# Performance work log

Measured on AMD Instinct MI355X. Metric: run time of the kernel, lower is better.

The kernel has to match this reference:

```python
import jax, jax.numpy as jnp
import numpy as np

TREE_DEPTH = 3
CONSTANTS = jnp.array([-1.0, 0.0, 1.0], dtype=jnp.float32)


def setup_inputs() -> dict:
    key = jax.random.key(0)
    ks = jax.random.split(key, 5)
    B, S, D, W, SLOT = 2, 2048, 1024, 4096, 8
    C = SLOT + 3
    hidden = jax.random.normal(ks[0], (B, S, D), dtype=jnp.float32)
    slot_w = jax.random.normal(ks[1], (D, SLOT), dtype=jnp.float32) * (0.5 / np.sqrt(D))
    slot_b = jnp.zeros((SLOT,), dtype=jnp.float32)
    leaf_logits = jax.random.normal(ks[2], (W, 1 << TREE_DEPTH, C), dtype=jnp.float32) * 0.02
    node_params = jnp.array([1.0, 1.0, 0.25, 0.0, 0.0], dtype=jnp.float32)
    out_w = jax.random.normal(ks[3], (W, D), dtype=jnp.float32) * (0.5 / np.sqrt(W))
    out_b = jnp.zeros((D,), dtype=jnp.float32)
    return {"hidden": hidden, "slot_w": slot_w, "slot_b": slot_b,
            "leaf_logits": leaf_logits, "node_params": node_params,
            "out_w": out_w, "out_b": out_b}


def reference(hidden, slot_w, slot_b, leaf_logits, node_params, out_w, out_b):
    B, S, _ = hidden.shape
    # basis: tanh slot projection concatenated with fixed constants -> [B,S,slot+3]
    slots = jnp.tanh(hidden @ slot_w + slot_b)
    consts = jnp.broadcast_to(CONSTANTS.astype(hidden.dtype), (B, S, 3))
    basis = jnp.concatenate((slots, consts), axis=-1)
    # leaf values: softmax-weighted mixture over the tiny basis dim -> [B,S,W,leaf]
    selector = jax.nn.softmax(leaf_logits.astype(hidden.dtype), axis=-1)
    values = jnp.einsum('wlc,bsc->bswl', selector, basis)
    lw, rw, pw, dw, nb = [p.astype(hidden.dtype) for p in node_params]
    for _ in range(TREE_DEPTH):
        left, right = values[..., 0::2], values[..., 1::2]
        values = jnp.tanh(lw * left + rw * right + pw * left * right
                          + dw * (left - right) + nb)
    roots = values[..., 0]  # [B,S,W]
    return roots @ out_w + out_b
```

## Files before the change

kernel.cpp:

```cpp
#include <hip/hip_runtime.h>
#include <stdint.h>

#define BSZ   4096
#define DIM   1024
#define WTR   4096
#define KDIM  4096
#define W8    32768

typedef unsigned short u16;
typedef __attribute__((ext_vector_type(8))) short bhalf8;
typedef __attribute__((ext_vector_type(4))) float floatx4;
typedef __attribute__((ext_vector_type(16))) float floatx16;

__device__ __forceinline__ u16 f2bf(float f) {
    union { float f; uint32_t i; } v; v.f = f;
    uint32_t r = v.i + 0x7fffu + ((v.i >> 16) & 1u);
    return (u16)(r >> 16);
}
__device__ __forceinline__ float fast_tanh(float x) {
    float e = __builtin_amdgcn_exp2f(x * 2.885390081777927f);
    return fmaf(-2.0f, __builtin_amdgcn_rcpf(e + 1.0f), 1.0f);
}
__device__ __forceinline__ void load16(const void* g, void* lds) {
    __builtin_amdgcn_global_load_lds(
        (const __attribute__((address_space(1))) uint32_t*)g,
        (__attribute__((address_space(3))) uint32_t*)lds, 16, 0, 0);
}

__global__ __launch_bounds__(256) void k_prep(const float* __restrict__ ll,
                                              u16* __restrict__ selwA,
                                              const float* __restrict__ ow,
                                              u16* __restrict__ owt,
                                              const float* __restrict__ slot_w,
                                              u16* __restrict__ swT) {
    int bid = blockIdx.x, tid = threadIdx.x;
    if (bid < 128) {
        int row = bid * 256 + tid;
        int w = row >> 3, l = row & 7, q = w & 3;
        int prow = (w >> 2) * 32 + (l & 3) + 8 * (l >> 2) + 16 * (q & 1) + 4 * (q >> 1);
        const float* p = ll + (size_t)row * 11;
        float v[11]; float m = -1e30f;
        #pragma unroll
        for (int c = 0; c < 11; ++c) { v[c] = p[c]; m = fmaxf(m, v[c]); }
        float s = 0.f;
        #pragma unroll
        for (int c = 0; c < 11; ++c) {
            v[c] = __builtin_amdgcn_exp2f((v[c] - m) * 1.4426950408889634f);
            s += v[c];
        }
        float inv = __builtin_amdgcn_rcpf(s);
        union { u16 h[16]; uint4 qq[2]; } o;
        #pragma unroll
        for (int c = 0; c < 8; ++c) o.h[c] = f2bf(v[c] * inv);
        o.h[8] = f2bf((v[10] - v[8]) * inv);
        #pragma unroll
        for (int c = 9; c < 16; ++c) o.h[c] = 0;
        uint4* dst = (uint4*)(selwA + (size_t)prow * 16);
        dst[0] = o.qq[0]; dst[1] = o.qq[1];
    } else if (bid < 128 + 4096) {
        int b = bid - 128;
        int d0 = (b & 31) * 32, w0 = (b >> 5) * 32;
        int tx = tid & 31, ty = tid >> 5;
        __shared__ float tile[32][33];
        #pragma unroll
        for (int i = 0; i < 32; i += 8)
            tile[ty + i][tx] = ow[(size_t)(w0 + ty + i) * DIM + d0 + tx];
        __syncthreads();
        #pragma unroll
        for (int i = 0; i < 32; i += 8)
            owt[(size_t)(d0 + ty + i) * WTR + w0 + tx] = f2bf(tile[tx][ty + i]);
    } else {
        int b = bid - 128 - 4096;
        for (int it = 0; it < 8; ++it) {
            int idx = b * 2048 + it * 256 + tid;
            int s = idx >> 10, d = idx & 1023;
            float val = (s < 8) ? slot_w[(size_t)d * 8 + s] : 0.f;
            swT[(size_t)s * DIM + d] = f2bf(val);
        }
    }
}

__global__ __launch_bounds__(256) void k_basis(const float* __restrict__ hidden,
                                               const u16* __restrict__ swT,
                                               const float* __restrict__ slot_b,
                                               u16* __restrict__ basisTB) {
    int m0 = blockIdx.x * 16;
    int tid = threadIdx.x, lane = tid & 63, wid = tid >> 6;
    int col = lane & 15, quad = lane >> 4;
    const float* ga = hidden + (size_t)(m0 + col) * DIM + wid * 256 + quad * 8;
    const u16*   gb = swT + (size_t)col * DIM + wid * 256 + quad * 8;
    floatx4 acc = (floatx4){0.f, 0.f, 0.f, 0.f};
    #pragma unroll
    for (int k0 = 0; k0 < 256; k0 += 32) {
        float4 a0 = *(const float4*)(ga + k0);
        float4 a1 = *(const float4*)(ga + k0 + 4);
        bhalf8 bf = *(const bhalf8*)(gb + k0);
        bhalf8 af;
        af[0] = (short)f2bf(a0.x); af[1] = (short)f2bf(a0.y);
        af[2] = (short)f2bf(a0.z); af[3] = (short)f2bf(a0.w);
        af[4] = (short)f2bf(a1.x); af[5] = (short)f2bf(a1.y);
        af[6] = (short)f2bf(a1.z); af[7] = (short)f2bf(a1.w);
        acc = __builtin_amdgcn_mfma_f32_16x16x32_bf16(af, bf, acc, 0, 0, 0);
    }
    __shared__ float smr[4][16][16];
    #pragma unroll
    for (int r = 0; r < 4; ++r) smr[wid][quad * 4 + r][col] = acc[r];
    __syncthreads();
    int tt = tid >> 4, cc = tid & 15;
    float s = smr[0][tt][cc] + smr[1][tt][cc] + smr[2][tt][cc] + smr[3][tt][cc];
    u16 val;
    if (cc < 8)       val = f2bf(fast_tanh(s + slot_b[cc]));
    else if (cc == 8) val = (u16)0x3f80;
    else              val = 0;
    basisTB[(size_t)(m0 + tt) * 16 + cc] = val;
}

__device__ __forceinline__ float tree_eval(float v[8], float lw, float rw,
                                           float pw, float dw, float nb) {
    #pragma unroll
    for (int lev = 0; lev < 3; ++lev) {
        int n = 4 >> lev;
        #pragma unroll
        for (int i = 0; i < 4; ++i) {
            if (i < n) {
                float L = v[2*i], R = v[2*i+1];
                float x = fmaf(lw, L, nb);
                x = fmaf(rw, R, x);
                x = fmaf(pw, L * R, x);
                x = fmaf(dw, L - R, x);
                v[i] = fast_tanh(x);
            }
        }
    }
    return v[0];
}

__global__ __launch_bounds__(256, 2) void k_roots(const u16* __restrict__ selwA,
                                                  const u16* __restrict__ basisTB,
                                                  const float* __restrict__ np_,
                                                  u16* __restrict__ roots) {
    __shared__ uint32_t st[4][32 * 12];
    int tid = threadIdx.x, wid = tid >> 6, lane = tid & 63;
    int c = lane & 31, h = lane >> 5;
    int tile0 = blockIdx.x * 16 + wid * 4;
    int w0w   = tile0 * 4;
    int t0b   = blockIdx.y * 512;
    float lw = np_[0], rw = np_[1], pw = np_[2], dw = np_[3], nb = np_[4];

    bhalf8 af[4];
    #pragma unroll
    for (int tl = 0; tl < 4; ++tl)
        af[tl] = *(const bhalf8*)(selwA + (size_t)((tile0 + tl) * 32 + c) * 16 + h * 8);

    uint32_t* myst = st[wid];
    for (int it = 0; it < 16; ++it) {
        int t0 = t0b + it * 32;
        bhalf8 bf = *(const bhalf8*)(basisTB + (size_t)(t0 + c) * 16 + h * 8);
        #pragma unroll
        for (int tl = 0; tl < 4; ++tl) {
            floatx16 z = {0.f,0.f,0.f,0.f,0.f,0.f,0.f,0.f,
                          0.f,0.f,0.f,0.f,0.f,0.f,0.f,0.f};
            floatx16 cc = __builtin_amdgcn_mfma_f32_32x32x16_bf16(af[tl], bf, z, 0, 0, 0);
            float vA[8], vB[8];
            #pragma unroll
            for (int l = 0; l < 8; ++l) { vA[l] = cc[l]; vB[l] = cc[8 + l]; }
            float rA = tree_eval(vA, lw, rw, pw, dw, nb);
            float rB = tree_eval(vB, lw, rw, pw, dw, nb);
            myst[c * 12 + tl * 2 + h] = (uint32_t)f2bf(rA) | ((uint32_t)f2bf(rB) << 16);
        }
        __syncthreads();
        uint4 q = *(const uint4*)(myst + c * 12 + h * 4);
        *(uint4*)(roots + (size_t)(t0 + c) * WTR + w0w + h * 8) = q;
        __syncthreads();
    }
}

__global__ __launch_bounds__(256) void k_gemm(const u16* __restrict__ A,
                                              const u16* __restrict__ Bt,
                                              const float* __restrict__ out_b,
                                              float* __restrict__ C) {
    __shared__ __align__(16) u16 smA[2][64 * 64];
    __shared__ __align__(16) u16 smB[2][128 * 64];
    int tid = threadIdx.x;
    int bm = blockIdx.x * 64, bn = blockIdx.y * 128;
    int lane = tid & 63, wid = tid >> 6;
    int wm = (wid >> 1) * 32, wn = (wid & 1) * 64;

    floatx4 acc[2][4];
    #pragma unroll
    for (int i = 0; i < 2; ++i)
        #pragma unroll
        for (int j = 0; j < 4; ++j) acc[i][j] = (floatx4){0.f, 0.f, 0.f, 0.f};

    int ar = tid >> 3;
    int ak = ((tid & 7) ^ (ar & 7)) * 8;
    const u16* gA = A  + (size_t)(bm + ar) * KDIM + ak;
    const u16* gB = Bt + (size_t)(bn + ar) * KDIM + ak;

    int col = lane & 15, quad = lane >> 4, csw = col & 7;

    {
        char* ldA = (char*)smA[0] + tid * 16;
        char* ldB = (char*)smB[0] + tid * 16;
        load16(gA,                       ldA);
        load16(gA + (size_t)32 * KDIM,   ldA + 4096);
        load16(gB,                       ldB);
        load16(gB + (size_t)32 * KDIM,   ldB + 4096);
        load16(gB + (size_t)64 * KDIM,   ldB + 8192);
        load16(gB + (size_t)96 * KDIM,   ldB + 12288);
        gA += 64; gB += 64;
    }

    int cur = 0;
    for (int k0 = 0; k0 < KDIM / 64; ++k0) {
        __syncthreads();
        if (k0 < KDIM / 64 - 1) {
            char* ldA = (char*)smA[cur ^ 1] + tid * 16;
            char* ldB = (char*)smB[cur ^ 1] + tid * 16;
            load16(gA,                       ldA);
            load16(gA + (size_t)32 * KDIM,   ldA + 4096);
            load16(gB,                       ldB);
            load16(gB + (size_t)32 * KDIM,   ldB + 4096);
            load16(gB + (size_t)64 * KDIM,   ldB + 8192);
            load16(gB + (size_t)96 * KDIM,   ldB + 12288);
            gA += 64; gB += 64;
        }
        const u16* sa = smA[cur];
        const u16* sb = smB[cur];
        #pragma unroll
        for (int kk = 0; kk < 2; ++kk) {
            int kc = kk * 4 + quad;
            bhalf8 af[2], bf[4];
            #pragma unroll
            for (int i = 0; i < 2; ++i)
                af[i] = *(const bhalf8*)(sa + ((wm + i * 16 + col) * 8 + (kc ^ csw)) * 8);
            #pragma unroll
            for (int j = 0; j < 4; ++j)
                bf[j] = *(const bhalf8*)(sb + ((wn + j * 16 + col) * 8 + (kc ^ csw)) * 8);
            #pragma unroll
            for (int i = 0; i < 2; ++i)
                #pragma unroll
                for (int j = 0; j < 4; ++j)
                    acc[i][j] = __builtin_amdgcn_mfma_f32_16x16x32_bf16(
                        af[i], bf[j], acc[i][j], 0, 0, 0);
        }
        cur ^= 1;
    }

    #pragma unroll
    for (int j = 0; j < 4; ++j) {
        int n = bn + wn + j * 16 + col;
        float bv = out_b[n];
        #pragma unroll
        for (int i = 0; i < 2; ++i) {
            int m0 = bm + wm + i * 16 + quad * 4;
            #pragma unroll
            for (int r = 0; r < 4; ++r)
                C[(size_t)(m0 + r) * DIM + n] = acc[i][j][r] + bv;
        }
    }
}

extern "C" void kernel_launch(void* const* d_in, const int* in_sizes, int n_in,
                              void* d_out, int out_size, void* d_ws, size_t ws_size,
                              hipStream_t stream) {
    const float* hidden      = (const float*)d_in[0];
    const float* slot_w      = (const float*)d_in[1];
    const float* slot_b      = (const float*)d_in[2];
    const float* leaf_logits = (const float*)d_in[3];
    const float* node_params = (const float*)d_in[4];
    const float* out_w       = (const float*)d_in[5];
    const float* out_b       = (const float*)d_in[6];
    float* out = (float*)d_out;

    char* ws = (char*)d_ws;
    u16* selwA   = (u16*)ws;
    u16* basisTB = (u16*)(ws + 1048576);
    u16* swT     = (u16*)(ws + 1179648);
    u16* outwt   = (u16*)(ws + 1212416);
    u16* roots   = (u16*)(ws + 9601024);

    k_prep <<<128 + 4096 + 8, 256, 0, stream>>>(leaf_logits, selwA, out_w, outwt, slot_w, swT);
    k_basis<<<BSZ / 16, 256, 0, stream>>>(hidden, swT, slot_b, basisTB);
    k_roots<<<dim3(64, 8), 256, 0, stream>>>(selwA, basisTB, node_params, roots);
    k_gemm <<<dim3(BSZ / 64, DIM / 128), 256, 0, stream>>>(roots, outwt, out_b, out);
}
```

Measured before the change: 206.8 us.

## Split-K final GEMM with atomic accumulation and coalesce roots stores

The output GEMM is split into two K halves across grid z, and each half accumulates into an output that k_prep pre-initializes with the bias, using atomicAdd. The GEMM drops LDS double buffering in favor of a single buffer with two barriers per step. k_roots now stages all four waves' results into a shared padded, double-buffered LDS tile, so each token row is written as one contiguous 128-byte segment and one barrier per iteration is removed. The aim is more blocks in flight for the GEMM and better-coalesced stores, at the cost of atomic traffic, nondeterministic summation order and less load/compute overlap in the GEMM.

```diff
diff --git a/kernel.cpp b/kernel.cpp
--- a/kernel.cpp
+++ b/kernel.cpp
@@ -32,7 +32,9 @@
                                               const float* __restrict__ ow,
                                               u16* __restrict__ owt,
                                               const float* __restrict__ slot_w,
-                                              u16* __restrict__ swT) {
+                                              u16* __restrict__ swT,
+                                              const float* __restrict__ out_b,
+                                              float* __restrict__ C) {
     int bid = blockIdx.x, tid = threadIdx.x;
     if (bid < 128) {
         int row = bid * 256 + tid;
@@ -69,13 +71,21 @@
         #pragma unroll
         for (int i = 0; i < 32; i += 8)
             owt[(size_t)(d0 + ty + i) * WTR + w0 + tx] = f2bf(tile[tx][ty + i]);
-    } else {
+    } else if (bid < 128 + 4096 + 8) {
         int b = bid - 128 - 4096;
         for (int it = 0; it < 8; ++it) {
             int idx = b * 2048 + it * 256 + tid;
             int s = idx >> 10, d = idx & 1023;
             float val = (s < 8) ? slot_w[(size_t)d * 8 + s] : 0.f;
             swT[(size_t)s * DIM + d] = f2bf(val);
+        }
+    } else {
+        int b = bid - 128 - 4096 - 8;
+        float4 bv = *(const float4*)(out_b + (tid & 255) * 4);
+        #pragma unroll
+        for (int it = 0; it < 16; ++it) {
+            size_t flat = (size_t)b * 16384 + it * 1024 + (tid & 255) * 4;
+            *(float4*)(C + flat) = bv;
         }
     }
 }
@@ -139,11 +149,11 @@
                                                   const u16* __restrict__ basisTB,
                                                   const float* __restrict__ np_,
                                                   u16* __restrict__ roots) {
-    __shared__ uint32_t st[4][32 * 12];
+    __shared__ uint32_t st[2][32 * 33];
     int tid = threadIdx.x, wid = tid >> 6, lane = tid & 63;
     int c = lane & 31, h = lane >> 5;
     int tile0 = blockIdx.x * 16 + wid * 4;
-    int w0w   = tile0 * 4;
+    int wblk  = blockIdx.x * 64;
     int t0b   = blockIdx.y * 512;
     float lw = np_[0], rw = np_[1], pw = np_[2], dw = np_[3], nb = np_[4];
 
@@ -152,9 +162,10 @@
     for (int tl = 0; tl < 4; ++tl)
         af[tl] = *(const bhalf8*)(selwA + (size_t)((tile0 + tl) * 32 + c) * 16 + h * 8);
 
-    uint32_t* myst = st[wid];
+    int tok = tid >> 3, ch = tid & 7;
     for (int it = 0; it < 16; ++it) {
         int t0 = t0b + it * 32;
+        uint32_t* buf = st[it & 1];
         bhalf8 bf = *(const bhalf8*)(basisTB + (size_t)(t0 + c) * 16 + h * 8);
         #pragma unroll
         for (int tl = 0; tl < 4; ++tl) {
@@ -166,23 +177,27 @@
             for (int l = 0; l < 8; ++l) { vA[l] = cc[l]; vB[l] = cc[8 + l]; }
             float rA = tree_eval(vA, lw, rw, pw, dw, nb);
             float rB = tree_eval(vB, lw, rw, pw, dw, nb);
-            myst[c * 12 + tl * 2 + h] = (uint32_t)f2bf(rA) | ((uint32_t)f2bf(rB) << 16);
-        }
-        __syncthreads();
-        uint4 q = *(const uint4*)(myst + c * 12 + h * 4);
-        *(uint4*)(roots + (size_t)(t0 + c) * WTR + w0w + h * 8) = q;
-        __syncthreads();
+            buf[c * 33 + wid * 8 + tl * 2 + h] =
+                (uint32_t)f2bf(rA) | ((uint32_t)f2bf(rB) << 16);
+        }
+        __syncthreads();
+        uint32_t d0 = buf[tok * 33 + ch * 4];
+        uint32_t d1 = buf[tok * 33 + ch * 4 + 1];
+        uint32_t d2 = buf[tok * 33 + ch * 4 + 2];
+        uint32_t d3 = buf[tok * 33 + ch * 4 + 3];
+        uint4 q; q.x = d0; q.y = d1; q.z = d2; q.w = d3;
+        *(uint4*)(roots + (size_t)(t0 + tok) * WTR + wblk + ch * 8) = q;
     }
 }
 
 __global__ __launch_bounds__(256) void k_gemm(const u16* __restrict__ A,
                                               const u16* __restrict__ Bt,
-                                              const float* __restrict__ out_b,
                                               float* __restrict__ C) {
-    __shared__ __align__(16) u16 smA[2][64 * 64];
-    __shared__ __align__(16) u16 smB[2][128 * 64];
+    __shared__ __align__(16) u16 smA[64 * 64];
+    __shared__ __align__(16) u16 smB[128 * 64];
     int tid = threadIdx.x;
     int bm = blockIdx.x * 64, bn = blockIdx.y * 128;
+    int koff = blockIdx.z * (KDIM / 2);
     int lane = tid & 63, wid = tid >> 6;
     int wm = (wid >> 1) * 32, wn = (wid & 1) * 64;
 
@@ -194,14 +209,15 @@
 
     int ar = tid >> 3;
     int ak = ((tid & 7) ^ (ar & 7)) * 8;
-    const u16* gA = A  + (size_t)(bm + ar) * KDIM + ak;
-    const u16* gB = Bt + (size_t)(bn + ar) * KDIM + ak;
+    const u16* gA = A  + (size_t)(bm + ar) * KDIM + koff + ak;
+    const u16* gB = Bt + (size_t)(bn + ar) * KDIM + koff + ak;
+    char* ldA = (char*)smA + tid * 16;
+    char* ldB = (char*)smB + tid * 16;
 
     int col = lane & 15, quad = lane >> 4, csw = col & 7;
 
-    {
-        char* ldA = (char*)smA[0] + tid * 16;
-        char* ldB = (char*)smB[0] + tid * 16;
+    for (int k0 = 0; k0 < KDIM / 2 / 64; ++k0) {
+        __syncthreads();
         load16(gA,                       ldA);
         load16(gA + (size_t)32 * KDIM,   ldA + 4096);
         load16(gB,                       ldB);
@@ -209,34 +225,18 @@
         load16(gB + (size_t)64 * KDIM,   ldB + 8192);
         load16(gB + (size_t)96 * KDIM,   ldB + 12288);
         gA += 64; gB += 64;
-    }
-
-    int cur = 0;
-    for (int k0 = 0; k0 < KDIM / 64; ++k0) {
-        __syncthreads();
-        if (k0 < KDIM / 64 - 1) {
-            char* ldA = (char*)smA[cur ^ 1] + tid * 16;
-            char* ldB = (char*)smB[cur ^ 1] + tid * 16;
-            load16(gA,                       ldA);
-            load16(gA + (size_t)32 * KDIM,   ldA + 4096);
-            load16(gB,                       ldB);
-            load16(gB + (size_t)32 * KDIM,   ldB + 4096);
-            load16(gB + (size_t)64 * KDIM,   ldB + 8192);
-            load16(gB + (size_t)96 * KDIM,   ldB + 12288);
-            gA += 64; gB += 64;
-        }
-        const u16* sa = smA[cur];
-        const u16* sb = smB[cur];
+        __syncthreads();
+
         #pragma unroll
         for (int kk = 0; kk < 2; ++kk) {
             int kc = kk * 4 + quad;
             bhalf8 af[2], bf[4];
             #pragma unroll
             for (int i = 0; i < 2; ++i)
-                af[i] = *(const bhalf8*)(sa + ((wm + i * 16 + col) * 8 + (kc ^ csw)) * 8);
+                af[i] = *(const bhalf8*)(smA + ((wm + i * 16 + col) * 8 + (kc ^ csw)) * 8);
             #pragma unroll
             for (int j = 0; j < 4; ++j)
-                bf[j] = *(const bhalf8*)(sb + ((wn + j * 16 + col) * 8 + (kc ^ csw)) * 8);
+                bf[j] = *(const bhalf8*)(smB + ((wn + j * 16 + col) * 8 + (kc ^ csw)) * 8);
             #pragma unroll
             for (int i = 0; i < 2; ++i)
                 #pragma unroll
@@ -244,19 +244,17 @@
                     acc[i][j] = __builtin_amdgcn_mfma_f32_16x16x32_bf16(
                         af[i], bf[j], acc[i][j], 0, 0, 0);
         }
-        cur ^= 1;
     }
 
     #pragma unroll
     for (int j = 0; j < 4; ++j) {
         int n = bn + wn + j * 16 + col;
-        float bv = out_b[n];
         #pragma unroll
         for (int i = 0; i < 2; ++i) {
             int m0 = bm + wm + i * 16 + quad * 4;
             #pragma unroll
             for (int r = 0; r < 4; ++r)
-                C[(size_t)(m0 + r) * DIM + n] = acc[i][j][r] + bv;
+                atomicAdd(&C[(size_t)(m0 + r) * DIM + n], acc[i][j][r]);
         }
     }
 }
@@ -280,8 +278,9 @@
     u16* outwt   = (u16*)(ws + 1212416);
     u16* roots   = (u16*)(ws + 9601024);
 
-    k_prep <<<128 + 4096 + 8, 256, 0, stream>>>(leaf_logits, selwA, out_w, outwt, slot_w, swT);
+    k_prep <<<128 + 4096 + 8 + 256, 256, 0, stream>>>(leaf_logits, selwA, out_w, outwt,
+                                                      slot_w, swT, out_b, out);
     k_basis<<<BSZ / 16, 256, 0, stream>>>(hidden, swT, slot_b, basisTB);
     k_roots<<<dim3(64, 8), 256, 0, stream>>>(selwA, basisTB, node_params, roots);
-    k_gemm <<<dim3(BSZ / 64, DIM / 128), 256, 0, stream>>>(roots, outwt, out_b, out);
-}
+    k_gemm <<<dim3(BSZ / 64, DIM / 128, 2), 256, 0, stream>>>(roots, outwt, out);
+}
```

Result: no change. 205.1 us (-0.8%).
